# Performance work log

Hardware: AMD Instinct MI355X
Metric: run time of the kernel (lower is better)

The kernel has to match this reference:

```python
import jax, jax.numpy as jnp
import numpy as np

B, S, ENC = 64, 2048, 1024          # batch, encoder seq len, encoder feature dim
U, E_DIM, V_SZ = 512, 256, 50000    # dec_units, embedding_dim, vocab_size
IN_DIM = ENC + E_DIM                # LSTM input: [context ; token embedding]


def setup_inputs() -> dict:
    key = jax.random.key(0)
    ks = jax.random.split(key, 16)
    g = lambda k, shp, s=0.02: (jax.random.normal(k, shp, jnp.float32) * s)
    return {
        "x": jax.random.randint(ks[0], (B, 1), 0, V_SZ),
        "c_fwd": g(ks[1], (B, U), 0.1),
        "c_bwd": g(ks[2], (B, U), 0.1),
        "enc_output": jax.random.normal(ks[3], (B, S, ENC), jnp.float32),
        "emb": g(ks[4], (V_SZ, E_DIM)),
        "W1_w": g(ks[5], (ENC, U)), "W1_b": jnp.zeros((U,), jnp.float32),
        "W2_w": g(ks[6], (U, U)),   "W2_b": jnp.zeros((U,), jnp.float32),
        "W3_w": g(ks[7], (U, U)),   "W3_b": jnp.zeros((U,), jnp.float32),
        "V_w": g(ks[8], (U, 1)),    "V_b": jnp.zeros((1,), jnp.float32),
        "Kf": g(ks[9], (IN_DIM, 4 * U)),  "bf": jnp.zeros((4 * U,), jnp.float32),
        "Kb": g(ks[10], (IN_DIM, 4 * U)), "bb": jnp.zeros((4 * U,), jnp.float32),
        "fc_w": g(ks[11], (2 * U, V_SZ)), "fc_b": jnp.zeros((V_SZ,), jnp.float32),
    }


def _lstm_step_zero_state(xin, K, b):
    # Keras LSTM single step from zero (h0, c0): recurrent term vanishes.
    # Gate order in Keras kernel: i, f, c(g), o.
    z = xin @ K + b
    i, f, g, o = jnp.split(z, 4, axis=-1)
    i, o = jax.nn.sigmoid(i), jax.nn.sigmoid(o)  # f gate multiplies c0=0
    c = i * jnp.tanh(g)
    h = o * jnp.tanh(c)
    return h, c


def reference(x, c_fwd, c_bwd, enc_output, emb,
              W1_w, W1_b, W2_w, W2_b, W3_w, W3_b, V_w, V_b,
              Kf, bf, Kb, bb, fc_w, fc_b):
    # Bahdanau additive attention: score [B, S, 1]
    hidden_proj = (c_fwd @ W2_w + W2_b + c_bwd @ W3_w + W3_b)[:, None, :]  # [B,1,U]
    score = jnp.tanh(enc_output @ W1_w + W1_b + hidden_proj) @ V_w + V_b
    attn = jax.nn.softmax(score, axis=1)                 # softmax over S
    ctx = jnp.sum(attn * enc_output, axis=1)             # [B, ENC]

    xe = emb[x[:, 0]]                                    # [B, E_DIM]
    xin = jnp.concatenate([ctx, xe], axis=-1)            # [B, ENC+E_DIM]

    # Bidirectional LSTM over a length-1 sequence from zero initial state:
    # both directions see the same single timestep with separate weights.
    hf, cf = _lstm_step_zero_state(xin, Kf, bf)
    hb, cb = _lstm_step_zero_state(xin, Kb, bb)

    out = jnp.concatenate([hf, hb], axis=-1)             # [B, 2U]
    logits = out @ fc_w + fc_b                           # [B, vocab]
    return logits, hf, cf, hb, cb
```

## Files before the change

### kernel.cpp

```cpp
#include <hip/hip_runtime.h>

using u16 = unsigned short;
typedef float f32x4 __attribute__((ext_vector_type(4)));
typedef float f32x16 __attribute__((ext_vector_type(16)));
typedef __bf16 bf16x8 __attribute__((ext_vector_type(8)));
typedef u16 u16x8 __attribute__((ext_vector_type(8)));
typedef u16 u16x4 __attribute__((ext_vector_type(4)));

static constexpr int OF_HPB   = 262144;
static constexpr int OF_CTXP  = 294912;
static constexpr int OF_STATS = 2392064;
static constexpr int OF_XIN   = 2394112;
static constexpr int OF_ZPART = 2476032;
static constexpr int OF_HHL   = 3000320;
static constexpr size_t SCRATCH_FLOATS = 3065856;
static constexpr size_t SCRATCH_BYTES  = SCRATCH_FLOATS * 4ull;

__device__ __forceinline__ u16 f2bf(float f) {
  unsigned u = __float_as_uint(f);
  u += 0x7FFFu + ((u >> 16) & 1u);
  return (u16)(u >> 16);
}
__device__ __forceinline__ float bf2f(u16 u) {
  return __uint_as_float((unsigned)u << 16);
}
__device__ __forceinline__ float fast_tanh(float x) {
  x = fminf(fmaxf(x, -20.f), 20.f);
  float e = __expf(2.f * x);
  return (e - 1.f) / (e + 1.f);
}
__device__ __forceinline__ float fast_sig(float x) { return 1.f / (1.f + __expf(-x)); }

__global__ void k_prep_w1(const float* __restrict__ W1w, u16* __restrict__ w1p) {
  __shared__ float tile[16][516];
  const int t = threadIdx.x;
  const int ks = blockIdx.x;
  {
    int kk = t >> 4, u0 = (t & 15) * 32;
    const float* src = W1w + (size_t)(ks * 16 + kk) * 512 + u0;
    #pragma unroll
    for (int i = 0; i < 8; ++i)
      *(float4*)&tile[kk][u0 + i * 4] = *(const float4*)(src + i * 4);
  }
  __syncthreads();
  #pragma unroll
  for (int q = 0; q < 4; ++q) {
    int c = t + q * 256;
    int wv = c >> 6, l = c & 63;
    int u = wv * 32 + (l & 31), koct = l >> 5;
    u16x8 p;
    #pragma unroll
    for (int e = 0; e < 8; ++e) p[e] = f2bf(tile[koct * 8 + e][u]);
    *(u16x8*)(w1p + (size_t)ks * 8192 + (size_t)c * 8) = p;
  }
}

__global__ void k_prep_hp(const float* __restrict__ cf, const float* __restrict__ cb,
                          const float* __restrict__ W2w, const float* __restrict__ W2b,
                          const float* __restrict__ W3w, const float* __restrict__ W3b,
                          const float* __restrict__ W1b, float* __restrict__ hpb) {
  __shared__ float cfl[512], cbl[512];
  const int b = blockIdx.x, t = threadIdx.x;
  cfl[t] = cf[(size_t)b * 512 + t];       cfl[t + 256] = cf[(size_t)b * 512 + t + 256];
  cbl[t] = cb[(size_t)b * 512 + t];       cbl[t + 256] = cb[(size_t)b * 512 + t + 256];
  __syncthreads();
  const int u1 = t, u2 = t + 256;
  float a1 = W2b[u1] + W3b[u1] + W1b[u1];
  float a2 = W2b[u2] + W3b[u2] + W1b[u2];
  for (int k = 0; k < 512; ++k) {
    float c1 = cfl[k], c2 = cbl[k];
    const float* r2 = W2w + (size_t)k * 512;
    const float* r3 = W3w + (size_t)k * 512;
    a1 += c1 * r2[u1] + c2 * r3[u1];
    a2 += c1 * r2[u2] + c2 * r3[u2];
  }
  hpb[(size_t)b * 512 + u1] = a1;
  hpb[(size_t)b * 512 + u2] = a2;
}

__global__ void __launch_bounds__(1024, 8)
k_attn(const float* __restrict__ enc, const u16* __restrict__ w1p,
       const float* __restrict__ hpb, const float* __restrict__ Vw,
       const float* __restrict__ Vb, float* __restrict__ ctxp,
       float* __restrict__ stats) {
  __shared__ __align__(16) u16 smem[8448];

  const int t = threadIdx.x;
  const int bid = blockIdx.x;
  const int b = bid >> 5, tile = bid & 31;
  const size_t row0 = (size_t)b * 2048 + (size_t)tile * 64;

  const int l = t & 63, wv = t >> 6;

  const u16* bbase = w1p + (size_t)wv * 512 + (size_t)l * 8;

  const int sr = t >> 2, sh = (t >> 1) & 1, sq = t & 1;
  const float* a_src = enc + (row0 + sr) * 1024 + sh * 8 + sq * 4;
  const int a_dst = ((sr >> 5) * 64 + (sr & 31) + (sh << 5)) * 8 + sq * 4;

  f32x16 acc0, acc1;
  #pragma unroll
  for (int i = 0; i < 16; ++i) { acc0[i] = 0.f; acc1[i] = 0.f; }

  float4 av0 = {0.f,0.f,0.f,0.f}, av1 = {0.f,0.f,0.f,0.f};
  if (t < 256) {
    float4 p0 = *(const float4*)(a_src);
    u16x4 w4;
    w4[0] = f2bf(p0.x); w4[1] = f2bf(p0.y); w4[2] = f2bf(p0.z); w4[3] = f2bf(p0.w);
    *(u16x4*)(smem + a_dst) = w4;
    av0 = *(const float4*)(a_src + 16);
    av1 = *(const float4*)(a_src + 32);
  }
  bf16x8 bcur = *(const bf16x8*)(bbase);
  asm volatile("s_waitcnt lgkmcnt(0)" ::: "memory");
  __builtin_amdgcn_s_barrier();
  __builtin_amdgcn_sched_barrier(0);

  #pragma unroll 2
  for (int ks = 0; ks < 64; ++ks) {
    const int cur = ks & 1;
    if (t < 256 && ks < 63) {
      u16x4 w4;
      w4[0] = f2bf(av0.x); w4[1] = f2bf(av0.y); w4[2] = f2bf(av0.z); w4[3] = f2bf(av0.w);
      *(u16x4*)(smem + ((cur ^ 1) << 10) + a_dst) = w4;
      av0 = av1;
      if (ks < 61) av1 = *(const float4*)(a_src + (ks + 3) * 16);
    }
    bf16x8 bnxt = bcur;
    if (ks < 63) bnxt = *(const bf16x8*)(bbase + (size_t)(ks + 1) * 8192);
    const u16* Ac = smem + (cur << 10);
    bf16x8 a0 = *(const bf16x8*)(Ac + l * 8);
    bf16x8 a1 = *(const bf16x8*)(Ac + 512 + l * 8);
    acc0 = __builtin_amdgcn_mfma_f32_32x32x16_bf16(a0, bcur, acc0, 0, 0, 0);
    acc1 = __builtin_amdgcn_mfma_f32_32x32x16_bf16(a1, bcur, acc1, 0, 0, 0);
    bcur = bnxt;
    asm volatile("s_waitcnt lgkmcnt(0)" ::: "memory");
    __builtin_amdgcn_s_barrier();
    __builtin_amdgcn_sched_barrier(0);
  }

  float* fsm = (float*)smem;
  float* red = fsm;
  float* scv = fsm + 1088;
  float* pcv = fsm + 1152;

  const int ucol = (wv << 5) + (l & 31);
  const float vwv = Vw[ucol];
  const float hpv = hpb[(size_t)b * 512 + ucol];
  const int hi4 = (l >> 5) * 4;
  const bool writer = ((l & 31) == 0);
  #pragma unroll
  for (int im = 0; im < 2; ++im) {
    #pragma unroll
    for (int r = 0; r < 16; ++r) {
      float s = vwv * fast_tanh((im ? acc1[r] : acc0[r]) + hpv);
      s += __shfl_xor(s, 1);
      s += __shfl_xor(s, 2);
      s += __shfl_xor(s, 4);
      s += __shfl_xor(s, 8);
      s += __shfl_xor(s, 16);
      if (writer) {
        int sl = im * 32 + (r & 3) + 8 * (r >> 2) + hi4;
        red[sl * 17 + wv] = s;
      }
    }
  }
  __syncthreads();
  if (t < 64) {
    float s = Vb[0];
    #pragma unroll
    for (int wq = 0; wq < 16; ++wq) s += red[t * 17 + wq];
    float e = __expf(s);
    scv[t] = e;
    float p = e;
    p += __shfl_xor(p, 1);  p += __shfl_xor(p, 2);  p += __shfl_xor(p, 4);
    p += __shfl_xor(p, 8);  p += __shfl_xor(p, 16); p += __shfl_xor(p, 32);
    if (t == 0) stats[bid] = p;
  }
  __syncthreads();

  {
    const int c4 = (t & 255) * 4;
    const int rq = t >> 8;
    const float* ep = enc + (row0 + rq * 16) * 1024 + c4;
    float ax = 0.f, ay = 0.f, az = 0.f, aw2 = 0.f;
    #pragma unroll 4
    for (int r = 0; r < 16; ++r) {
      float4 v = *(const float4*)(ep + (size_t)r * 1024);
      float sc = scv[rq * 16 + r];
      ax += sc * v.x; ay += sc * v.y; az += sc * v.z; aw2 += sc * v.w;
    }
    if (rq) {
      float4 st = {ax, ay, az, aw2};
      *(float4*)&pcv[(rq - 1) * 1024 + c4] = st;
    }
    __syncthreads();
    if (rq == 0) {
      float4 p1 = *(const float4*)&pcv[c4];
      float4 p2 = *(const float4*)&pcv[1024 + c4];
      float4 p3 = *(const float4*)&pcv[2048 + c4];
      float4 o = {ax + p1.x + p2.x + p3.x, ay + p1.y + p2.y + p3.y,
                  az + p1.z + p2.z + p3.z, aw2 + p1.w + p2.w + p3.w};
      *(float4*)&ctxp[(size_t)bid * 1024 + c4] = o;
    }
  }
}

__global__ void k_attn_reduce(const float* __restrict__ ctxp, const float* __restrict__ stats,
                              const int* __restrict__ x, const float* __restrict__ emb,
                              float* __restrict__ xin) {
  __shared__ float ps[32];
  __shared__ float invs;
  const int b = blockIdx.x, t = threadIdx.x;
  if (t < 32) ps[t] = stats[b * 32 + t];
  __syncthreads();
  if (t == 0) {
    float s = 0.f;
    #pragma unroll
    for (int i = 0; i < 32; ++i) s += ps[i];
    invs = 1.f / s;
  }
  __syncthreads();
  const float inv = invs;
  #pragma unroll
  for (int i = 0; i < 4; ++i) {
    int c = t + i * 256;
    float a = 0.f;
    for (int chv = 0; chv < 32; ++chv)
      a += ctxp[((size_t)b * 32 + chv) * 1024 + c];
    xin[(size_t)b * 1280 + c] = a * inv;
  }
  xin[(size_t)b * 1280 + 1024 + t] = emb[(size_t)x[b] * 256 + t];
}

__global__ void k_lstm_gemm(const float* __restrict__ xin, const float* __restrict__ Kf,
                            const float* __restrict__ Kb, float* __restrict__ zpart) {
  __shared__ float xl[32][68];
  const int t = threadIdx.x;
  const int bid = blockIdx.x;
  const int dir = bid >> 7;
  const int jt  = (bid >> 1) & 63;
  const int ks  = bid & 1;
  const float* K = dir ? Kb : Kf;
  const int j  = jt * 32 + (t & 31);
  const int tb = t >> 5;
  const int brow = t >> 2, kq = (t & 3) * 8;
  float acc[8] = {0,0,0,0,0,0,0,0};
  for (int k0 = ks * 640; k0 < ks * 640 + 640; k0 += 32) {
    float4 x0 = *(const float4*)&xin[(size_t)brow * 1280 + k0 + kq];
    float4 x1 = *(const float4*)&xin[(size_t)brow * 1280 + k0 + kq + 4];
    __syncthreads();
    xl[kq+0][brow]=x0.x; xl[kq+1][brow]=x0.y; xl[kq+2][brow]=x0.z; xl[kq+3][brow]=x0.w;
    xl[kq+4][brow]=x1.x; xl[kq+5][brow]=x1.y; xl[kq+6][brow]=x1.z; xl[kq+7][brow]=x1.w;
    __syncthreads();
    const float* Kp = K + (size_t)k0 * 2048 + j;
    #pragma unroll 8
    for (int kk = 0; kk < 32; ++kk) {
      float wv = Kp[(size_t)kk * 2048];
      float4 v0 = *(const float4*)&xl[kk][tb * 8];
      float4 v1 = *(const float4*)&xl[kk][tb * 8 + 4];
      acc[0] += v0.x * wv; acc[1] += v0.y * wv; acc[2] += v0.z * wv; acc[3] += v0.w * wv;
      acc[4] += v1.x * wv; acc[5] += v1.y * wv; acc[6] += v1.z * wv; acc[7] += v1.w * wv;
    }
  }
  float* zp = zpart + ((size_t)dir * 2 + ks) * 64 * 2048;
  #pragma unroll
  for (int i = 0; i < 8; ++i)
    zp[(size_t)(tb * 8 + i) * 2048 + j] = acc[i];
}

__global__ void k_gates(const float* __restrict__ zpart, const float* __restrict__ bfv,
                        const float* __restrict__ bbv, float* __restrict__ dout,
                        u16* __restrict__ hhl) {
  const int dir = blockIdx.x >> 6, b = blockIdx.x & 63, u = threadIdx.x;
  const float* bias = dir ? bbv : bfv;
  const float* z0 = zpart + ((size_t)dir * 2 + 0) * 131072 + (size_t)b * 2048;
  const float* z1 = zpart + ((size_t)dir * 2 + 1) * 131072 + (size_t)b * 2048;
  float zi = z0[u]        + z1[u]        + bias[u];
  float zg = z0[1024 + u] + z1[1024 + u] + bias[1024 + u];
  float zo = z0[1536 + u] + z1[1536 + u] + bias[1536 + u];
  float c = fast_sig(zi) * fast_tanh(zg);
  float h = fast_sig(zo) * fast_tanh(c);
  size_t base = 3200000u + (size_t)dir * 65536u;
  dout[base + (size_t)b * 512 + u] = h;
  dout[base + 32768u + (size_t)b * 512 + u] = c;
  u16 hi = f2bf(h);
  u16 lo = f2bf(h - bf2f(hi));
  hhl[(size_t)b * 1024 + dir * 512 + u] = hi;
  hhl[65536u + (size_t)b * 1024 + dir * 512 + u] = lo;
}

__global__ void __launch_bounds__(256)
k_fc_mfma(const float* __restrict__ fcw, const u16* __restrict__ hhl,
          const float* __restrict__ fcb, float* __restrict__ logits) {
  __shared__ float Bs[2][32 * 136];
  const int t = threadIdx.x;
  const int j0 = blockIdx.x * 128;
  const int l = t & 63, w = t >> 6;
  const int ln = l & 15, lg = l >> 4;
  const int srow = t >> 3, scol = (t & 7) * 16;
  const bool interior = (j0 + 128 <= 50000);

  f32x4 acc[4][2];
  #pragma unroll
  for (int im = 0; im < 4; ++im)
    #pragma unroll
    for (int nf = 0; nf < 2; ++nf) acc[im][nf] = f32x4{0.f, 0.f, 0.f, 0.f};

  float4 pre[4];
  {
    const float* src = fcw + (size_t)srow * 50000 + j0 + scol;
    if (interior) {
      #pragma unroll
      for (int q = 0; q < 4; ++q) pre[q] = *(const float4*)(src + q * 4);
    } else {
      #pragma unroll
      for (int q = 0; q < 4; ++q) {
        int jb = j0 + scol + q * 4;
        pre[q].x = (jb + 0 < 50000) ? src[q*4 + 0] : 0.f;
        pre[q].y = (jb + 1 < 50000) ? src[q*4 + 1] : 0.f;
        pre[q].z = (jb + 2 < 50000) ? src[q*4 + 2] : 0.f;
        pre[q].w = (jb + 3 < 50000) ? src[q*4 + 3] : 0.f;
      }
    }
    #pragma unroll
    for (int q = 0; q < 4; ++q)
      *(float4*)&Bs[0][srow * 136 + scol + q * 4] = pre[q];
  }
  __syncthreads();

  for (int ks = 0; ks < 32; ++ks) {
    const int cur = ks & 1;
    if (ks < 31) {
      const float* src = fcw + (size_t)(ks + 1) * 32 * 50000 + (size_t)srow * 50000 + j0 + scol;
      if (interior) {
        #pragma unroll
        for (int q = 0; q < 4; ++q) pre[q] = *(const float4*)(src + q * 4);
      } else {
        #pragma unroll
        for (int q = 0; q < 4; ++q) {
          int jb = j0 + scol + q * 4;
          pre[q].x = (jb + 0 < 50000) ? src[q*4 + 0] : 0.f;
          pre[q].y = (jb + 1 < 50000) ? src[q*4 + 1] : 0.f;
          pre[q].z = (jb + 2 < 50000) ? src[q*4 + 2] : 0.f;
          pre[q].w = (jb + 3 < 50000) ? src[q*4 + 3] : 0.f;
        }
      }
    }
    bf16x8 ahi[4], alo[4];
    #pragma unroll
    for (int im = 0; im < 4; ++im) {
      const u16* ha = hhl + (size_t)(im * 16 + ln) * 1024 + ks * 32 + lg * 8;
      ahi[im] = *(const bf16x8*)(ha);
      alo[im] = *(const bf16x8*)(ha + 65536);
    }
    bf16x8 bfr[2];
    #pragma unroll
    for (int nf = 0; nf < 2; ++nf) {
      u16x8 pv;
      #pragma unroll
      for (int i = 0; i < 8; ++i)
        pv[i] = f2bf(Bs[cur][(lg * 8 + i) * 136 + w * 32 + nf * 16 + ln]);
      bfr[nf] = *(bf16x8*)&pv;
    }
    #pragma unroll
    for (int im = 0; im < 4; ++im)
      #pragma unroll
      for (int nf = 0; nf < 2; ++nf) {
        acc[im][nf] = __builtin_amdgcn_mfma_f32_16x16x32_bf16(alo[im], bfr[nf], acc[im][nf], 0, 0, 0);
        acc[im][nf] = __builtin_amdgcn_mfma_f32_16x16x32_bf16(ahi[im], bfr[nf], acc[im][nf], 0, 0, 0);
      }
    if (ks < 31) {
      #pragma unroll
      for (int q = 0; q < 4; ++q)
        *(float4*)&Bs[cur ^ 1][srow * 136 + scol + q * 4] = pre[q];
    }
    __syncthreads();
  }

  #pragma unroll
  for (int nf = 0; nf < 2; ++nf) {
    int c = j0 + w * 32 + nf * 16 + ln;
    if (c < 50000) {
      float fb = fcb[c];
      #pragma unroll
      for (int im = 0; im < 4; ++im)
        #pragma unroll
        for (int r = 0; r < 4; ++r) {
          int row = im * 16 + lg * 4 + r;
          logits[(size_t)row * 50000 + c] = acc[im][nf][r] + fb;
        }
    }
  }
}

__global__ void __launch_bounds__(256)
k_fc_f32(const float* __restrict__ dout_ro, const float* __restrict__ fcw,
         const float* __restrict__ fcb, float* __restrict__ logits) {
  __shared__ float ol[64][68];
  __shared__ float wl[64][132];
  const int t = threadIdx.x;
  const int j0 = blockIdx.x * 128;
  const int tb = t >> 5, tj = t & 31;
  const float* hf = dout_ro + 3200000u;
  const float* hb = dout_ro + 3200000u + 65536u;
  float acc[8][4];
  #pragma unroll
  for (int bi = 0; bi < 8; ++bi)
    #pragma unroll
    for (int ji = 0; ji < 4; ++ji) acc[bi][ji] = 0.f;

  for (int k0 = 0; k0 < 1024; k0 += 64) {
    __syncthreads();
    {
      int bb = t >> 2, kq = (t & 3) * 16;
      const float* src = (k0 < 512) ? (hf + (size_t)bb * 512 + k0 + kq)
                                    : (hb + (size_t)bb * 512 + (k0 - 512) + kq);
      #pragma unroll
      for (int i = 0; i < 4; ++i) {
        float4 v = *(const float4*)(src + i * 4);
        ol[kq + i*4 + 0][bb] = v.x;
        ol[kq + i*4 + 1][bb] = v.y;
        ol[kq + i*4 + 2][bb] = v.z;
        ol[kq + i*4 + 3][bb] = v.w;
      }
    }
    {
      int kk = t >> 2, jh = (t & 3) * 32;
      const float* wsrc = fcw + (size_t)(k0 + kk) * 50000 + j0 + jh;
      #pragma unroll
      for (int i = 0; i < 8; ++i) {
        int j = j0 + jh + i * 4;
        float4 v;
        if (j + 3 < 50000) {
          v = *(const float4*)(wsrc + i * 4);
        } else {
          v.x = (j + 0 < 50000) ? wsrc[i*4 + 0] : 0.f;
          v.y = (j + 1 < 50000) ? wsrc[i*4 + 1] : 0.f;
          v.z = (j + 2 < 50000) ? wsrc[i*4 + 2] : 0.f;
          v.w = 0.f;
        }
        *(float4*)&wl[kk][jh + i * 4] = v;
      }
    }
    __syncthreads();
    #pragma unroll 4
    for (int kk = 0; kk < 64; ++kk) {
      float4 wv = *(const float4*)&wl[kk][tj * 4];
      float4 q0 = *(const float4*)&ol[kk][tb * 8];
      float4 q1 = *(const float4*)&ol[kk][tb * 8 + 4];
      float obv[8] = {q0.x, q0.y, q0.z, q0.w, q1.x, q1.y, q1.z, q1.w};
      #pragma unroll
      for (int bi = 0; bi < 8; ++bi) {
        acc[bi][0] += obv[bi] * wv.x;
        acc[bi][1] += obv[bi] * wv.y;
        acc[bi][2] += obv[bi] * wv.z;
        acc[bi][3] += obv[bi] * wv.w;
      }
    }
  }

  const int j = j0 + tj * 4;
  if (j + 3 < 50000) {
    float4 fb = *(const float4*)(fcb + j);
    #pragma unroll
    for (int bi = 0; bi < 8; ++bi) {
      float4 r;
      r.x = acc[bi][0] + fb.x; r.y = acc[bi][1] + fb.y;
      r.z = acc[bi][2] + fb.z; r.w = acc[bi][3] + fb.w;
      *(float4*)&logits[(size_t)(tb * 8 + bi) * 50000 + j] = r;
    }
  } else {
    for (int ji = 0; ji < 4; ++ji) {
      if (j + ji < 50000) {
        float fb = fcb[j + ji];
        for (int bi = 0; bi < 8; ++bi)
          logits[(size_t)(tb * 8 + bi) * 50000 + j + ji] = acc[bi][ji] + fb;
      }
    }
  }
}

extern "C" void kernel_launch(void* const* d_in, const int* in_sizes, int n_in,
                              void* d_out, int out_size, void* d_ws, size_t ws_size,
                              hipStream_t stream) {
  const int*   x    = (const int*)  d_in[0];
  const float* cfwd = (const float*)d_in[1];
  const float* cbwd = (const float*)d_in[2];
  const float* enc  = (const float*)d_in[3];
  const float* emb  = (const float*)d_in[4];
  const float* W1w  = (const float*)d_in[5];
  const float* W1b  = (const float*)d_in[6];
  const float* W2w  = (const float*)d_in[7];
  const float* W2b  = (const float*)d_in[8];
  const float* W3w  = (const float*)d_in[9];
  const float* W3b  = (const float*)d_in[10];
  const float* Vw   = (const float*)d_in[11];
  const float* Vb   = (const float*)d_in[12];
  const float* Kf   = (const float*)d_in[13];
  const float* bfv  = (const float*)d_in[14];
  const float* Kb   = (const float*)d_in[15];
  const float* bbv  = (const float*)d_in[16];
  const float* fcw  = (const float*)d_in[17];
  const float* fcb  = (const float*)d_in[18];
  float* out = (float*)d_out;

  const bool haveWs = (ws_size >= SCRATCH_BYTES);
  float* S = haveWs ? (float*)d_ws : out;
  u16*   w1p   = (u16*)S;
  float* hpb   = S + OF_HPB;
  float* ctxp  = S + OF_CTXP;
  float* stats = S + OF_STATS;
  float* xin   = S + OF_XIN;
  float* zpart = S + OF_ZPART;
  u16*   hhl   = (u16*)(S + OF_HHL);

  k_prep_w1<<<64, 256, 0, stream>>>(W1w, w1p);
  k_prep_hp<<<64, 256, 0, stream>>>(cfwd, cbwd, W2w, W2b, W3w, W3b, W1b, hpb);
  k_attn<<<2048, 1024, 0, stream>>>(enc, w1p, hpb, Vw, Vb, ctxp, stats);
  k_attn_reduce<<<64, 256, 0, stream>>>(ctxp, stats, x, emb, xin);
  k_lstm_gemm<<<256, 256, 0, stream>>>(xin, Kf, Kb, zpart);
  k_gates<<<128, 512, 0, stream>>>(zpart, bfv, bbv, out, hhl);
  if (haveWs) k_fc_mfma<<<392, 256, 0, stream>>>(fcw, hhl, fcb, out);
  else        k_fc_f32<<<391, 256, 0, stream>>>(out, fcw, fcb, out);
}
```

Before: 540.5 us.

## Stage four K-slices per barrier in attention GEMM main loop

The attention score GEMM loop now stages 64 K-columns of the encoder tile per iteration, using all 1024 threads for the fp32-to-bf16 conversion, instead of 16 columns per iteration loaded by 256 threads. It runs 16 barrier-separated iterations of four MFMA pairs each instead of 64 iterations of one pair. The aim is to cut barrier and waitcnt overhead and to widen global load parallelism. The LDS sub-tiles are padded (stride 1032) to avoid bank conflicts. The cost is a larger shared buffer footprint. The W1 fragments are also now loaded synchronously inside each iteration rather than prefetched, which may expose their latency.

```diff
diff --git a/kernel.cpp b/kernel.cpp
--- a/kernel.cpp
+++ b/kernel.cpp
@@ -94,46 +94,49 @@
 
   const u16* bbase = w1p + (size_t)wv * 512 + (size_t)l * 8;
 
-  const int sr = t >> 2, sh = (t >> 1) & 1, sq = t & 1;
-  const float* a_src = enc + (row0 + sr) * 1024 + sh * 8 + sq * 4;
-  const int a_dst = ((sr >> 5) * 64 + (sr & 31) + (sh << 5)) * 8 + sq * 4;
+  const int sr = t >> 4, sq4 = t & 15;
+  const float* a_src = enc + (row0 + sr) * 1024 + sq4 * 4;
+  const int sm = sq4 >> 2, skoct = (sq4 >> 1) & 1, ssq = sq4 & 1;
+  const int a_dst = sm * 1032 + (sr >> 5) * 512 + ((sr & 31) + skoct * 32) * 8 + ssq * 4;
 
   f32x16 acc0, acc1;
   #pragma unroll
   for (int i = 0; i < 16; ++i) { acc0[i] = 0.f; acc1[i] = 0.f; }
 
-  float4 av0 = {0.f,0.f,0.f,0.f}, av1 = {0.f,0.f,0.f,0.f};
-  if (t < 256) {
-    float4 p0 = *(const float4*)(a_src);
+  float4 pv0, pv1;
+  {
+    float4 v = *(const float4*)(a_src);
     u16x4 w4;
-    w4[0] = f2bf(p0.x); w4[1] = f2bf(p0.y); w4[2] = f2bf(p0.z); w4[3] = f2bf(p0.w);
+    w4[0] = f2bf(v.x); w4[1] = f2bf(v.y); w4[2] = f2bf(v.z); w4[3] = f2bf(v.w);
     *(u16x4*)(smem + a_dst) = w4;
-    av0 = *(const float4*)(a_src + 16);
-    av1 = *(const float4*)(a_src + 32);
-  }
-  bf16x8 bcur = *(const bf16x8*)(bbase);
+    pv0 = *(const float4*)(a_src + 64);
+    pv1 = *(const float4*)(a_src + 128);
+  }
   asm volatile("s_waitcnt lgkmcnt(0)" ::: "memory");
   __builtin_amdgcn_s_barrier();
   __builtin_amdgcn_sched_barrier(0);
 
-  #pragma unroll 2
-  for (int ks = 0; ks < 64; ++ks) {
-    const int cur = ks & 1;
-    if (t < 256 && ks < 63) {
+  for (int km = 0; km < 16; ++km) {
+    const int cur = km & 1;
+    if (km < 15) {
       u16x4 w4;
-      w4[0] = f2bf(av0.x); w4[1] = f2bf(av0.y); w4[2] = f2bf(av0.z); w4[3] = f2bf(av0.w);
-      *(u16x4*)(smem + ((cur ^ 1) << 10) + a_dst) = w4;
-      av0 = av1;
-      if (ks < 61) av1 = *(const float4*)(a_src + (ks + 3) * 16);
-    }
-    bf16x8 bnxt = bcur;
-    if (ks < 63) bnxt = *(const bf16x8*)(bbase + (size_t)(ks + 1) * 8192);
-    const u16* Ac = smem + (cur << 10);
-    bf16x8 a0 = *(const bf16x8*)(Ac + l * 8);
-    bf16x8 a1 = *(const bf16x8*)(Ac + 512 + l * 8);
-    acc0 = __builtin_amdgcn_mfma_f32_32x32x16_bf16(a0, bcur, acc0, 0, 0, 0);
-    acc1 = __builtin_amdgcn_mfma_f32_32x32x16_bf16(a1, bcur, acc1, 0, 0, 0);
-    bcur = bnxt;
+      w4[0] = f2bf(pv0.x); w4[1] = f2bf(pv0.y); w4[2] = f2bf(pv0.z); w4[3] = f2bf(pv0.w);
+      *(u16x4*)(smem + (cur ^ 1) * 4128 + a_dst) = w4;
+      pv0 = pv1;
+      if (km < 13) pv1 = *(const float4*)(a_src + (km + 3) * 64);
+    }
+    bf16x8 bfr[4];
+    #pragma unroll
+    for (int m = 0; m < 4; ++m)
+      bfr[m] = *(const bf16x8*)(bbase + (size_t)(km * 4 + m) * 8192);
+    const u16* Ac = smem + cur * 4128;
+    #pragma unroll
+    for (int m = 0; m < 4; ++m) {
+      bf16x8 a0 = *(const bf16x8*)(Ac + m * 1032 + l * 8);
+      bf16x8 a1 = *(const bf16x8*)(Ac + m * 1032 + 512 + l * 8);
+      acc0 = __builtin_amdgcn_mfma_f32_32x32x16_bf16(a0, bfr[m], acc0, 0, 0, 0);
+      acc1 = __builtin_amdgcn_mfma_f32_32x32x16_bf16(a1, bfr[m], acc1, 0, 0, 0);
+    }
     asm volatile("s_waitcnt lgkmcnt(0)" ::: "memory");
     __builtin_amdgcn_s_barrier();
     __builtin_amdgcn_sched_barrier(0);
```

After: 508.5 us. -5.9%, faster.
